# Kernel optimization log

Hardware: AMD Instinct MI355X
Metric: run time of the kernel (lower is better)

## Reference

```python
import jax, jax.numpy as jnp
import numpy as np

V, K, NB = 200000, 24, 10
P = K * 9  # pose-blendshape feature dim = 216
# Standard SMPL/STAR kinematic tree; root's parent set to itself (handled specially).
PARENTS = np.array([0, 0, 0, 0, 1, 2, 3, 4, 5, 6, 7, 8, 9, 9, 9, 12, 13, 14, 16, 17, 18, 19, 20, 21])


def setup_inputs() -> dict:
    key = jax.random.key(0)
    ks = jax.random.split(key, 7)
    return {
        "betas": jax.random.normal(ks[0], (NB,), dtype=jnp.float32),
        "pose": jax.random.normal(ks[1], (K * 3,), dtype=jnp.float32),
        "v_template": jax.random.normal(ks[2], (V, 3), dtype=jnp.float32),
        "shapedirs": jax.random.normal(ks[3], (V, 3, NB), dtype=jnp.float32) * 0.01,
        "posedirs": jax.random.normal(ks[4], (V, 3, P), dtype=jnp.float32) * 0.01,
        "J_regressor": jax.random.uniform(ks[5], (K, V), dtype=jnp.float32) / V,
        "weights": jax.random.uniform(ks[6], (V, K), dtype=jnp.float32),
    }


def _rodrigues(r):
    # r: (K,3) axis-angle -> (K,3,3) rotation matrices (matches torch version incl. +1e-12)
    theta = jnp.linalg.norm(r + 1e-12, axis=1, keepdims=True)  # (K,1)
    k = r / theta
    kx, ky, kz = k[:, 0], k[:, 1], k[:, 2]
    z = jnp.zeros_like(kx)
    Km = jnp.stack([z, -kz, ky, kz, z, -kx, -ky, kx, z], axis=1).reshape(-1, 3, 3)
    s = jnp.sin(theta)[:, :, None]
    c = jnp.cos(theta)[:, :, None]
    return jnp.eye(3, dtype=r.dtype) + s * Km + (1.0 - c) * (Km @ Km)


def reference(betas, pose, v_template, shapedirs, posedirs, J_regressor, weights):
    # shape blendshapes
    v_shaped = v_template + jnp.einsum('vci,i->vc', shapedirs, betas)  # (V,3)
    J = J_regressor @ v_shaped  # (K,3) joint locations in rest pose
    R = _rodrigues(pose.reshape(K, 3))  # (K,3,3)
    # pose blendshapes: features are (R - I) flattened over all K joints
    pose_feat = (R - jnp.eye(3, dtype=R.dtype)).reshape(-1)  # (K*9,)
    v_posed = v_shaped + jnp.einsum('vcp,p->vc', posedirs, pose_feat)
    # relative joint translations along the kinematic chain
    rel = J - J[PARENTS]
    rel = rel.at[0].set(J[0])
    # forward kinematics: A[j] = A[parent] @ [[R_j, rel_j],[0,1]]  (K=24, unrolled)
    A_rot = [R[0]]
    A_t = [rel[0]]
    for j in range(1, K):
        p = int(PARENTS[j])
        A_rot.append(A_rot[p] @ R[j])
        A_t.append(A_rot[p] @ rel[j] + A_t[p])
    rot = jnp.stack(A_rot)  # (K,3,3)
    # T[k] = A[k] @ inv(A_rest[k]); A_rest is pure translation by J[k], so
    # T_rot = rot, T_trans = A_t - rot @ J  (analytic inverse of translation)
    trans = jnp.stack(A_t) - jnp.einsum('kij,kj->ki', rot, J)  # (K,3)
    # LBS: blend transforms per vertex (avoids dense K x V x 4 intermediate)
    W_rot = jnp.einsum('vk,kij->vij', weights, rot)  # (V,3,3)
    W_t = weights @ trans  # (V,3)
    return jnp.einsum('vij,vj->vi', W_rot, v_posed) + W_t  # (V,3)
```

## Files before the change

kernel.cpp:

```cpp
#include <hip/hip_runtime.h>

#define NV 200000
#define NPAIR 100000
#define NK 24
#define NCH 64

#define PART_OFF 0
#define J_OFF    4608
#define ROT_OFF  4680
#define TR_OFF   4896
#define PF_OFF   4968

template <int CTRL>
__device__ __forceinline__ float dpp_add(float x) {
    int y = __builtin_amdgcn_update_dpp(0, __float_as_int(x), CTRL, 0xf, 0xf, true);
    return x + __int_as_float(y);
}

__global__ __launch_bounds__(256) void kA(const float* __restrict__ vt,
                                          const float* __restrict__ sd,
                                          const float* __restrict__ betas,
                                          float* __restrict__ vs_out) {
    int v = blockIdx.x * 256 + threadIdx.x;
    if (v >= NV) return;
    float b[10];
#pragma unroll
    for (int i = 0; i < 10; i++) b[i] = betas[i];
    size_t v3 = 3 * (size_t)v;
    float acc0 = vt[v3], acc1 = vt[v3 + 1], acc2 = vt[v3 + 2];
    const float2* s2 = (const float2*)(sd) + (size_t)v * 15;
#pragma unroll
    for (int j = 0; j < 15; j++) {
        float2 s = s2[j];
        const int e0 = 2 * j, e1 = 2 * j + 1;
        float p0 = s.x * b[e0 % 10];
        float p1 = s.y * b[e1 % 10];
        if (e0 / 10 == 0) acc0 += p0; else if (e0 / 10 == 1) acc1 += p0; else acc2 += p0;
        if (e1 / 10 == 0) acc0 += p1; else if (e1 / 10 == 1) acc1 += p1; else acc2 += p1;
    }
    vs_out[v3] = acc0; vs_out[v3 + 1] = acc1; vs_out[v3 + 2] = acc2;
}

__global__ __launch_bounds__(256) void kB(const float* __restrict__ jr,
                                          const float* __restrict__ vs,
                                          float* __restrict__ ws) {
    int k = blockIdx.x >> 6;
    int chunk = blockIdx.x & 63;
    const float* row = jr + (size_t)k * NV;
    float a0 = 0.f, a1 = 0.f, a2 = 0.f;
    for (int v = chunk * 256 + threadIdx.x; v < NV; v += NCH * 256) {
        float w = row[v];
        size_t v3 = 3 * (size_t)v;
        a0 = fmaf(w, vs[v3], a0);
        a1 = fmaf(w, vs[v3 + 1], a1);
        a2 = fmaf(w, vs[v3 + 2], a2);
    }
#pragma unroll
    for (int off = 32; off; off >>= 1) {
        a0 += __shfl_xor(a0, off, 64);
        a1 += __shfl_xor(a1, off, 64);
        a2 += __shfl_xor(a2, off, 64);
    }
    __shared__ float red[4][3];
    int lane = threadIdx.x & 63, wv = threadIdx.x >> 6;
    if (lane == 0) { red[wv][0] = a0; red[wv][1] = a1; red[wv][2] = a2; }
    __syncthreads();
    if (threadIdx.x < 3) {
        float s = red[0][threadIdx.x] + red[1][threadIdx.x] +
                  red[2][threadIdx.x] + red[3][threadIdx.x];
        ws[PART_OFF + blockIdx.x * 3 + threadIdx.x] = s;
    }
}

__global__ __launch_bounds__(64) void kC(const float* __restrict__ pose,
                                         float* __restrict__ ws) {
    __shared__ float Jl[72];
    __shared__ float Rl[24][9];
    __shared__ float Ar[24][9];
    __shared__ float At[24][3];
    int t = threadIdx.x;

    for (int idx = t; idx < 72; idx += 64) {
        int k = idx / 3, c = idx % 3;
        float s = 0.f;
#pragma unroll
        for (int ch = 0; ch < NCH; ch++) s += ws[PART_OFF + (k * NCH + ch) * 3 + c];
        Jl[idx] = s;
    }

    if (t < 24) {
        float rx = pose[3 * t], ry = pose[3 * t + 1], rz = pose[3 * t + 2];
        float tx = rx + 1e-12f, ty = ry + 1e-12f, tz = rz + 1e-12f;
        float th = sqrtf(tx * tx + ty * ty + tz * tz);
        float inv = 1.0f / th;
        float kx = rx * inv, ky = ry * inv, kz = rz * inv;
        float s = sinf(th), c = cosf(th), oc = 1.0f - c;
        float R00 = 1.f + oc * (-(ky * ky + kz * kz));
        float R01 = -s * kz + oc * kx * ky;
        float R02 =  s * ky + oc * kx * kz;
        float R10 =  s * kz + oc * kx * ky;
        float R11 = 1.f + oc * (-(kx * kx + kz * kz));
        float R12 = -s * kx + oc * ky * kz;
        float R20 = -s * ky + oc * kx * kz;
        float R21 =  s * kx + oc * ky * kz;
        float R22 = 1.f + oc * (-(kx * kx + ky * ky));
        Rl[t][0] = R00; Rl[t][1] = R01; Rl[t][2] = R02;
        Rl[t][3] = R10; Rl[t][4] = R11; Rl[t][5] = R12;
        Rl[t][6] = R20; Rl[t][7] = R21; Rl[t][8] = R22;
        float* pf = ws + PF_OFF + t * 9;
        pf[0] = R00 - 1.f; pf[1] = R01;       pf[2] = R02;
        pf[3] = R10;       pf[4] = R11 - 1.f; pf[5] = R12;
        pf[6] = R20;       pf[7] = R21;       pf[8] = R22 - 1.f;
    }
    __syncthreads();

    const int par[24] = {0,0,0,0,1,2,3,4,5,6,7,8,9,9,9,12,13,14,16,17,18,19,20,21};
    const int lvl[24] = {0,1,1,1,2,2,2,3,3,3,4,4,4,4,4,5,5,5,6,6,7,7,8,8};
    float rel0 = 0.f, rel1 = 0.f, rel2 = 0.f;
    int p = 0, myl = -1;
    if (t < 24) {
        p = par[t]; myl = lvl[t];
        if (t == 0) { rel0 = Jl[0]; rel1 = Jl[1]; rel2 = Jl[2]; }
        else {
            rel0 = Jl[3 * t]     - Jl[3 * p];
            rel1 = Jl[3 * t + 1] - Jl[3 * p + 1];
            rel2 = Jl[3 * t + 2] - Jl[3 * p + 2];
        }
    }
    for (int L = 0; L < 9; L++) {
        if (myl == L) {
            if (t == 0) {
#pragma unroll
                for (int e = 0; e < 9; e++) Ar[0][e] = Rl[0][e];
                At[0][0] = rel0; At[0][1] = rel1; At[0][2] = rel2;
            } else {
#pragma unroll
                for (int i = 0; i < 3; i++) {
                    float ai0 = Ar[p][i * 3], ai1 = Ar[p][i * 3 + 1], ai2 = Ar[p][i * 3 + 2];
#pragma unroll
                    for (int jj = 0; jj < 3; jj++) {
                        Ar[t][i * 3 + jj] = ai0 * Rl[t][jj] + ai1 * Rl[t][3 + jj] + ai2 * Rl[t][6 + jj];
                    }
                    At[t][i] = ai0 * rel0 + ai1 * rel1 + ai2 * rel2 + At[p][i];
                }
            }
        }
        __syncthreads();
    }
    if (t < 24) {
#pragma unroll
        for (int i = 0; i < 3; i++) {
            float tr = At[t][i] - (Ar[t][i * 3]     * Jl[3 * t] +
                                   Ar[t][i * 3 + 1] * Jl[3 * t + 1] +
                                   Ar[t][i * 3 + 2] * Jl[3 * t + 2]);
            ws[TR_OFF + t * 3 + i] = tr;
        }
#pragma unroll
        for (int e = 0; e < 9; e++) ws[ROT_OFF + t * 9 + e] = Ar[t][e];
    }
}

__global__ __launch_bounds__(256) void kD(const float* __restrict__ pd,
                                          const float* __restrict__ wts,
                                          const float* __restrict__ ws,
                                          float* __restrict__ out) {
    int t = threadIdx.x;
    int l = t & 63;

    const float4* pf4 = (const float4*)(ws + PF_OFF);
    float4 b0 = pf4[(l < 54) ? l      : l - 54];
    float4 b1 = pf4[(l < 44) ? l + 10 : l - 44];
    float4 b2 = pf4[(l < 34) ? l + 20 : l - 34];
    float4 b3 = pf4[(l < 24) ? l + 30 : l - 24];
    float4 b4 = pf4[(l < 14) ? l + 40 : l - 14];
    float4 b5 = pf4[(l <  4) ? l + 50 : 0];

    int h  = l >> 5;
    int kk = l & 31;
    float rr0=0,rr1=0,rr2=0,rr3=0,rr4=0,rr5=0,rr6=0,rr7=0,rr8=0;
    float tt0=0, tt1=0, tt2=0;
    if (kk < 24) {
        const float* r = ws + ROT_OFF + kk * 9;
        rr0=r[0]; rr1=r[1]; rr2=r[2]; rr3=r[3]; rr4=r[4];
        rr5=r[5]; rr6=r[6]; rr7=r[7]; rr8=r[8];
        const float* tr = ws + TR_OFF + kk * 3;
        tt0=tr[0]; tt1=tr[1]; tt2=tr[2];
    }

    int wid = (blockIdx.x << 2) + (t >> 6);
    int stride = gridDim.x << 2;
    for (int p = wid; p < NPAIR; p += stride) {
        const float4* base = (const float4*)(pd) + (size_t)p * 324;
        float4 A0 = base[l];
        float4 A1 = base[l + 64];
        float4 A2 = base[l + 128];
        float4 A3 = base[l + 192];
        float4 A4 = base[l + 256];
        float4 A5 = make_float4(0.f, 0.f, 0.f, 0.f);
        if (l < 4) A5 = base[l + 320];

        int vmy = 2 * p + h;
        const float* vsp = out + (size_t)vmy * 3;
        float vsx = vsp[0], vsy = vsp[1], vsz = vsp[2];
        float wk = (kk < 24) ? wts[(size_t)vmy * 24 + kk] : 0.f;

        float d0 = A0.x * b0.x + A0.y * b0.y + A0.z * b0.z + A0.w * b0.w;
        float d1 = A1.x * b1.x + A1.y * b1.y + A1.z * b1.z + A1.w * b1.w;
        float d2 = A2.x * b2.x + A2.y * b2.y + A2.z * b2.z + A2.w * b2.w;
        float d3 = A3.x * b3.x + A3.y * b3.y + A3.z * b3.z + A3.w * b3.w;
        float d4 = A4.x * b4.x + A4.y * b4.y + A4.z * b4.z + A4.w * b4.w;
        float d5 = A5.x * b5.x + A5.y * b5.y + A5.z * b5.z + A5.w * b5.w;

        float s0 = (l < 54) ? d0 : 0.f;
        float s1 = ((l < 54) ? 0.f : d0) + ((l < 44) ? d1 : 0.f);
        float s2 = ((l < 44) ? 0.f : d1) + ((l < 34) ? d2 : 0.f);
        float s3 = ((l < 34) ? 0.f : d2) + ((l < 24) ? d3 : 0.f);
        float s4 = ((l < 24) ? 0.f : d3) + ((l < 14) ? d4 : 0.f);
        float s5 = ((l < 14) ? 0.f : d4) + d5;

        s0 = dpp_add<0xB1>(s0); s1 = dpp_add<0xB1>(s1); s2 = dpp_add<0xB1>(s2);
        s3 = dpp_add<0xB1>(s3); s4 = dpp_add<0xB1>(s4); s5 = dpp_add<0xB1>(s5);
        s0 = dpp_add<0x4E>(s0); s1 = dpp_add<0x4E>(s1); s2 = dpp_add<0x4E>(s2);
        s3 = dpp_add<0x4E>(s3); s4 = dpp_add<0x4E>(s4); s5 = dpp_add<0x4E>(s5);
        s0 = dpp_add<0x141>(s0); s1 = dpp_add<0x141>(s1); s2 = dpp_add<0x141>(s2);
        s3 = dpp_add<0x141>(s3); s4 = dpp_add<0x141>(s4); s5 = dpp_add<0x141>(s5);
        s0 = dpp_add<0x140>(s0); s1 = dpp_add<0x140>(s1); s2 = dpp_add<0x140>(s2);
        s3 = dpp_add<0x140>(s3); s4 = dpp_add<0x140>(s4); s5 = dpp_add<0x140>(s5);
        s0 += __shfl_xor(s0, 16, 64); s1 += __shfl_xor(s1, 16, 64); s2 += __shfl_xor(s2, 16, 64);
        s3 += __shfl_xor(s3, 16, 64); s4 += __shfl_xor(s4, 16, 64); s5 += __shfl_xor(s5, 16, 64);
        s0 += __shfl_xor(s0, 32, 64); s1 += __shfl_xor(s1, 32, 64); s2 += __shfl_xor(s2, 32, 64);
        s3 += __shfl_xor(s3, 32, 64); s4 += __shfl_xor(s4, 32, 64); s5 += __shfl_xor(s5, 32, 64);

        float vpx = vsx + (h ? s3 : s0);
        float vpy = vsy + (h ? s4 : s1);
        float vpz = vsz + (h ? s5 : s2);

        float m0 = wk * (rr0 * vpx + rr1 * vpy + rr2 * vpz + tt0);
        float m1 = wk * (rr3 * vpx + rr4 * vpy + rr5 * vpz + tt1);
        float m2 = wk * (rr6 * vpx + rr7 * vpy + rr8 * vpz + tt2);

        m0 = dpp_add<0xB1>(m0); m1 = dpp_add<0xB1>(m1); m2 = dpp_add<0xB1>(m2);
        m0 = dpp_add<0x4E>(m0); m1 = dpp_add<0x4E>(m1); m2 = dpp_add<0x4E>(m2);
        m0 = dpp_add<0x141>(m0); m1 = dpp_add<0x141>(m1); m2 = dpp_add<0x141>(m2);
        m0 = dpp_add<0x140>(m0); m1 = dpp_add<0x140>(m1); m2 = dpp_add<0x140>(m2);
        m0 += __shfl_xor(m0, 16, 64); m1 += __shfl_xor(m1, 16, 64); m2 += __shfl_xor(m2, 16, 64);

        if (kk < 3) {
            out[(size_t)vmy * 3 + kk] = (kk == 0) ? m0 : (kk == 1) ? m1 : m2;
        }
    }
}

extern "C" void kernel_launch(void* const* d_in, const int* in_sizes, int n_in,
                              void* d_out, int out_size, void* d_ws, size_t ws_size,
                              hipStream_t stream) {
    const float* betas = (const float*)d_in[0];
    const float* pose  = (const float*)d_in[1];
    const float* vt    = (const float*)d_in[2];
    const float* sd    = (const float*)d_in[3];
    const float* pd    = (const float*)d_in[4];
    const float* jr    = (const float*)d_in[5];
    const float* wts   = (const float*)d_in[6];
    float* out = (float*)d_out;
    float* ws  = (float*)d_ws;

    kA<<<(NV + 255) / 256, 256, 0, stream>>>(vt, sd, betas, out);
    kB<<<NK * NCH, 256, 0, stream>>>(jr, out, ws);
    kC<<<1, 64, 0, stream>>>(pose, ws);
    kD<<<2048, 256, 0, stream>>>(pd, wts, ws, out);
}
```

Measured before the change: 125.9 us.

## Fuse shape blend with joint regression and software-pipeline posedirs loads

Merges the shape-blendshape kernel and the joint-regressor reduction into one kernel, so v_shaped is reduced against the 24 J_regressor rows while still in registers instead of being re-read from memory. Per-block partials are written to the workspace and kC, now run with 576 threads, reduces the 782 partials in two stages. kD moves from a grid-stride loop to a fixed 4 pairs per wave with double-buffered prefetch of the next pair's posedirs, v_shaped and weights, launched with 6250 blocks. This adds register pressure and a larger partial reduction in the single-block kC.

Measured after the change: 147.5 us. 17.1% more time.

```diff
diff --git a/kernel.cpp b/kernel.cpp
--- a/kernel.cpp
+++ b/kernel.cpp
@@ -3,13 +3,13 @@
 #define NV 200000
 #define NPAIR 100000
 #define NK 24
-#define NCH 64
+#define NBLK 782
 
 #define PART_OFF 0
-#define J_OFF    4608
-#define ROT_OFF  4680
-#define TR_OFF   4896
-#define PF_OFF   4968
+#define J_OFF    56304
+#define ROT_OFF  56376
+#define TR_OFF   56592
+#define PF_OFF   56664
 
 template <int CTRL>
 __device__ __forceinline__ float dpp_add(float x) {
@@ -17,77 +17,77 @@
     return x + __int_as_float(y);
 }
 
-__global__ __launch_bounds__(256) void kA(const float* __restrict__ vt,
-                                          const float* __restrict__ sd,
-                                          const float* __restrict__ betas,
-                                          float* __restrict__ vs_out) {
-    int v = blockIdx.x * 256 + threadIdx.x;
-    if (v >= NV) return;
-    float b[10];
-#pragma unroll
-    for (int i = 0; i < 10; i++) b[i] = betas[i];
-    size_t v3 = 3 * (size_t)v;
-    float acc0 = vt[v3], acc1 = vt[v3 + 1], acc2 = vt[v3 + 2];
-    const float2* s2 = (const float2*)(sd) + (size_t)v * 15;
-#pragma unroll
-    for (int j = 0; j < 15; j++) {
-        float2 s = s2[j];
-        const int e0 = 2 * j, e1 = 2 * j + 1;
-        float p0 = s.x * b[e0 % 10];
-        float p1 = s.y * b[e1 % 10];
-        if (e0 / 10 == 0) acc0 += p0; else if (e0 / 10 == 1) acc1 += p0; else acc2 += p0;
-        if (e1 / 10 == 0) acc0 += p1; else if (e1 / 10 == 1) acc1 += p1; else acc2 += p1;
-    }
-    vs_out[v3] = acc0; vs_out[v3 + 1] = acc1; vs_out[v3 + 2] = acc2;
-}
-
-__global__ __launch_bounds__(256) void kB(const float* __restrict__ jr,
-                                          const float* __restrict__ vs,
+__global__ __launch_bounds__(256) void kAB(const float* __restrict__ vt,
+                                           const float* __restrict__ sd,
+                                           const float* __restrict__ betas,
+                                           const float* __restrict__ jr,
+                                           float* __restrict__ out,
+                                           float* __restrict__ ws) {
+    int tid = threadIdx.x;
+    int v = blockIdx.x * 256 + tid;
+    bool ok = (v < NV);
+    float b10[10];
+#pragma unroll
+    for (int i = 0; i < 10; i++) b10[i] = betas[i];
+    float a0 = 0.f, a1 = 0.f, a2 = 0.f;
+    if (ok) {
+        size_t v3 = 3 * (size_t)v;
+        a0 = vt[v3]; a1 = vt[v3 + 1]; a2 = vt[v3 + 2];
+        const float2* s2 = (const float2*)(sd) + (size_t)v * 15;
+#pragma unroll
+        for (int j = 0; j < 15; j++) {
+            float2 s = s2[j];
+            const int e0 = 2 * j, e1 = 2 * j + 1;
+            float p0 = s.x * b10[e0 % 10];
+            float p1 = s.y * b10[e1 % 10];
+            if (e0 / 10 == 0) a0 += p0; else if (e0 / 10 == 1) a1 += p0; else a2 += p0;
+            if (e1 / 10 == 0) a0 += p1; else if (e1 / 10 == 1) a1 += p1; else a2 += p1;
+        }
+        out[v3] = a0; out[v3 + 1] = a1; out[v3 + 2] = a2;
+    }
+
+    __shared__ float red[24][4][3];
+    int l = tid & 63, w = tid >> 6;
+    for (int k = 0; k < 24; k++) {
+        float jw = ok ? jr[(size_t)k * NV + v] : 0.f;
+        float p0 = jw * a0, p1 = jw * a1, p2 = jw * a2;
+        p0 = dpp_add<0xB1>(p0);  p1 = dpp_add<0xB1>(p1);  p2 = dpp_add<0xB1>(p2);
+        p0 = dpp_add<0x4E>(p0);  p1 = dpp_add<0x4E>(p1);  p2 = dpp_add<0x4E>(p2);
+        p0 = dpp_add<0x141>(p0); p1 = dpp_add<0x141>(p1); p2 = dpp_add<0x141>(p2);
+        p0 = dpp_add<0x140>(p0); p1 = dpp_add<0x140>(p1); p2 = dpp_add<0x140>(p2);
+        p0 += __shfl_xor(p0, 16, 64); p1 += __shfl_xor(p1, 16, 64); p2 += __shfl_xor(p2, 16, 64);
+        p0 += __shfl_xor(p0, 32, 64); p1 += __shfl_xor(p1, 32, 64); p2 += __shfl_xor(p2, 32, 64);
+        if (l == 0) { red[k][w][0] = p0; red[k][w][1] = p1; red[k][w][2] = p2; }
+    }
+    __syncthreads();
+    if (tid < 72) {
+        int k = tid / 3, c = tid % 3;
+        float s = red[k][0][c] + red[k][1][c] + red[k][2][c] + red[k][3][c];
+        ws[PART_OFF + (size_t)blockIdx.x * 72 + tid] = s;
+    }
+}
+
+__global__ __launch_bounds__(576) void kC(const float* __restrict__ pose,
                                           float* __restrict__ ws) {
-    int k = blockIdx.x >> 6;
-    int chunk = blockIdx.x & 63;
-    const float* row = jr + (size_t)k * NV;
-    float a0 = 0.f, a1 = 0.f, a2 = 0.f;
-    for (int v = chunk * 256 + threadIdx.x; v < NV; v += NCH * 256) {
-        float w = row[v];
-        size_t v3 = 3 * (size_t)v;
-        a0 = fmaf(w, vs[v3], a0);
-        a1 = fmaf(w, vs[v3 + 1], a1);
-        a2 = fmaf(w, vs[v3 + 2], a2);
-    }
-#pragma unroll
-    for (int off = 32; off; off >>= 1) {
-        a0 += __shfl_xor(a0, off, 64);
-        a1 += __shfl_xor(a1, off, 64);
-        a2 += __shfl_xor(a2, off, 64);
-    }
-    __shared__ float red[4][3];
-    int lane = threadIdx.x & 63, wv = threadIdx.x >> 6;
-    if (lane == 0) { red[wv][0] = a0; red[wv][1] = a1; red[wv][2] = a2; }
-    __syncthreads();
-    if (threadIdx.x < 3) {
-        float s = red[0][threadIdx.x] + red[1][threadIdx.x] +
-                  red[2][threadIdx.x] + red[3][threadIdx.x];
-        ws[PART_OFF + blockIdx.x * 3 + threadIdx.x] = s;
-    }
-}
-
-__global__ __launch_bounds__(64) void kC(const float* __restrict__ pose,
-                                         float* __restrict__ ws) {
+    __shared__ float part[8][72];
     __shared__ float Jl[72];
     __shared__ float Rl[24][9];
     __shared__ float Ar[24][9];
     __shared__ float At[24][3];
     int t = threadIdx.x;
-
-    for (int idx = t; idx < 72; idx += 64) {
-        int k = idx / 3, c = idx % 3;
+    int g = t / 72, idx = t - g * 72;
+    {
         float s = 0.f;
-#pragma unroll
-        for (int ch = 0; ch < NCH; ch++) s += ws[PART_OFF + (k * NCH + ch) * 3 + c];
-        Jl[idx] = s;
-    }
-
+        for (int b = g; b < NBLK; b += 8) s += ws[PART_OFF + (size_t)b * 72 + idx];
+        part[g][idx] = s;
+    }
+    __syncthreads();
+    if (t < 72) {
+        float s = 0.f;
+#pragma unroll
+        for (int gg = 0; gg < 8; gg++) s += part[gg][t];
+        Jl[t] = s;
+    }
     if (t < 24) {
         float rx = pose[3 * t], ry = pose[3 * t + 1], rz = pose[3 * t + 2];
         float tx = rx + 1e-12f, ty = ry + 1e-12f, tz = rz + 1e-12f;
@@ -187,22 +187,43 @@
         tt0=tr[0]; tt1=tr[1]; tt2=tr[2];
     }
 
-    int wid = (blockIdx.x << 2) + (t >> 6);
-    int stride = gridDim.x << 2;
-    for (int p = wid; p < NPAIR; p += stride) {
-        const float4* base = (const float4*)(pd) + (size_t)p * 324;
-        float4 A0 = base[l];
-        float4 A1 = base[l + 64];
-        float4 A2 = base[l + 128];
-        float4 A3 = base[l + 192];
-        float4 A4 = base[l + 256];
-        float4 A5 = make_float4(0.f, 0.f, 0.f, 0.f);
-        if (l < 4) A5 = base[l + 320];
-
-        int vmy = 2 * p + h;
-        const float* vsp = out + (size_t)vmy * 3;
-        float vsx = vsp[0], vsy = vsp[1], vsz = vsp[2];
-        float wk = (kk < 24) ? wts[(size_t)vmy * 24 + kk] : 0.f;
+    int gw = (blockIdx.x << 2) + (t >> 6);
+    int p0 = gw << 2;
+
+    const float4* base = (const float4*)(pd) + (size_t)p0 * 324;
+    float4 A0 = base[l];
+    float4 A1 = base[l + 64];
+    float4 A2 = base[l + 128];
+    float4 A3 = base[l + 192];
+    float4 A4 = base[l + 256];
+    float4 A5 = make_float4(0.f, 0.f, 0.f, 0.f);
+    if (l < 4) A5 = base[l + 320];
+    int vmy = 2 * p0 + h;
+    float vsx = out[(size_t)vmy * 3];
+    float vsy = out[(size_t)vmy * 3 + 1];
+    float vsz = out[(size_t)vmy * 3 + 2];
+    float wk = (kk < 24) ? wts[(size_t)vmy * 24 + kk] : 0.f;
+
+#pragma unroll
+    for (int i = 0; i < 4; i++) {
+        float4 N0 = A0, N1 = A1, N2 = A2, N3 = A3, N4 = A4, N5 = A5;
+        float nvsx = vsx, nvsy = vsy, nvsz = vsz, nwk = wk;
+        int nvmy = vmy;
+        if (i < 3) {
+            const float4* nb = (const float4*)(pd) + (size_t)(p0 + i + 1) * 324;
+            N0 = nb[l];
+            N1 = nb[l + 64];
+            N2 = nb[l + 128];
+            N3 = nb[l + 192];
+            N4 = nb[l + 256];
+            N5 = make_float4(0.f, 0.f, 0.f, 0.f);
+            if (l < 4) N5 = nb[l + 320];
+            nvmy = 2 * (p0 + i + 1) + h;
+            nvsx = out[(size_t)nvmy * 3];
+            nvsy = out[(size_t)nvmy * 3 + 1];
+            nvsz = out[(size_t)nvmy * 3 + 2];
+            nwk = (kk < 24) ? wts[(size_t)nvmy * 24 + kk] : 0.f;
+        }
 
         float d0 = A0.x * b0.x + A0.y * b0.y + A0.z * b0.z + A0.w * b0.w;
         float d1 = A1.x * b1.x + A1.y * b1.y + A1.z * b1.z + A1.w * b1.w;
@@ -248,6 +269,9 @@
         if (kk < 3) {
             out[(size_t)vmy * 3 + kk] = (kk == 0) ? m0 : (kk == 1) ? m1 : m2;
         }
+
+        A0 = N0; A1 = N1; A2 = N2; A3 = N3; A4 = N4; A5 = N5;
+        vsx = nvsx; vsy = nvsy; vsz = nvsz; wk = nwk; vmy = nvmy;
     }
 }
 
@@ -264,8 +288,7 @@
     float* out = (float*)d_out;
     float* ws  = (float*)d_ws;
 
-    kA<<<(NV + 255) / 256, 256, 0, stream>>>(vt, sd, betas, out);
-    kB<<<NK * NCH, 256, 0, stream>>>(jr, out, ws);
-    kC<<<1, 64, 0, stream>>>(pose, ws);
-    kD<<<2048, 256, 0, stream>>>(pd, wts, ws, out);
-}
+    kAB<<<NBLK, 256, 0, stream>>>(vt, sd, betas, jr, out, ws);
+    kC<<<1, 576, 0, stream>>>(pose, ws);
+    kD<<<6250, 256, 0, stream>>>(pd, wts, ws, out);
+}
```
